# Optimization experiments

Measured on AMD Instinct MI355X. Metric: run time of the kernel, lower is better.

Reference implementation:

```python
import jax, jax.numpy as jnp
import numpy as np

V_CNT = 10000
B = 16
N = B * V_CNT          # total nodes
K = 6                  # Chebyshev order
CH = [3, 128, 64, 32, 128]
G = 8                  # GroupNorm groups (divides 128, 64, 32)
EPS = 1e-5
AVG_DEG = 16


def setup_inputs() -> dict:
    key = jax.random.key(0)
    ks = jax.random.split(key, 8)
    n_edges = N * AVG_DEG
    inp = {
        "x": jax.random.normal(ks[0], (N, CH[0]), jnp.float32),
        "edge_index": jax.random.randint(ks[1], (2, n_edges), 0, N, jnp.int32).astype(jnp.int64),
    }
    for l in range(3):
        cin, cout = CH[l], CH[l + 1]
        s = (1.0 / (cin * K)) ** 0.5
        inp[f"W{l}"] = jax.random.uniform(ks[2 + l], (K, cin, cout), jnp.float32, -s, s)
        inp[f"b{l}"] = jnp.zeros((cout,), jnp.float32)
        inp[f"gamma{l}"] = jnp.ones((cout,), jnp.float32)
        inp[f"beta{l}"] = jnp.zeros((cout,), jnp.float32)
    din = V_CNT * CH[3]
    s = (1.0 / din) ** 0.5
    inp["W_last"] = jax.random.uniform(ks[5], (din, CH[4]), jnp.float32, -s, s)
    inp["b_last"] = jnp.zeros((CH[4],), jnp.float32)
    return inp


def _cheb_edge_weights(edge_index):
    # PyG ChebConv sym normalization with lambda_max=2: L_hat = L - I = -D^{-1/2} A D^{-1/2}
    row, col = edge_index[0], edge_index[1]
    deg = jax.ops.segment_sum(jnp.ones(row.shape, jnp.float32), row, num_segments=N)
    dis = jnp.where(deg > 0, jax.lax.rsqrt(jnp.maximum(deg, 1.0)), 0.0)  # deg^{-1/2}, inf->0
    return -dis[row] * dis[col], row, col


def _cheb_conv(x, row, col, w, W, b):
    # Chebyshev recursion: Tx0=x, Tx1=L_hat x, Tx_k = 2 L_hat Tx_{k-1} - Tx_{k-2}
    prop = lambda h: jax.ops.segment_sum(w[:, None] * h[col], row, num_segments=N)
    Tx0 = x
    out = Tx0 @ W[0]
    Tx1 = prop(Tx0)
    out = out + Tx1 @ W[1]
    for k in range(2, W.shape[0]):
        Tx2 = 2.0 * prop(Tx1) - Tx0
        out = out + Tx2 @ W[k]
        Tx0, Tx1 = Tx1, Tx2
    return out + b


def _group_norm(h, gamma, beta):
    n, C = h.shape
    hg = h.reshape(n, G, C // G)
    mu = hg.mean(axis=2, keepdims=True)
    var = hg.var(axis=2, keepdims=True)
    hg = (hg - mu) * jax.lax.rsqrt(var + EPS)
    return hg.reshape(n, C) * gamma + beta


def reference(x, edge_index, W0, b0, gamma0, beta0, W1, b1, gamma1, beta1,
              W2, b2, gamma2, beta2, W_last, b_last):
    w, row, col = _cheb_edge_weights(edge_index)
    Ws = [W0, W1, W2]
    bs = [b0, b1, b2]
    gs = [gamma0, gamma1, gamma2]
    betas = [beta0, beta1, beta2]
    h = x
    for l in range(3):
        h = _cheb_conv(h, row, col, w, Ws[l], bs[l])
        h = _group_norm(h, gs[l], betas[l])
        h = jax.nn.relu(h)
    h = h.reshape(-1, V_CNT * CH[3])  # [B, v_cnt*32]
    return h @ W_last + b_last
```

## Files before the change

kernel.cpp:

```cpp
#include <hip/hip_runtime.h>
#include <hip/hip_fp16.h>


#define NN 160000
#define EE 2560000
#define FD2 256
#define NBKT 625
#define BCAPL 13

typedef __attribute__((ext_vector_type(8))) _Float16 half8;
typedef __attribute__((ext_vector_type(4))) float floatx4;

__device__ inline float2 h2f2(unsigned u) {
  __half2 h = __builtin_bit_cast(__half2, u);
  return __half22float2(h);
}
__device__ inline unsigned short f2h(float f) {
  return __builtin_bit_cast(unsigned short, __float2half_rn(f));
}
__device__ inline unsigned packh2(float a, float b) {
  return __builtin_bit_cast(unsigned, __floats2half2_rn(a, b));
}

__global__ __launch_bounds__(256) void k_zero(int* __restrict__ p, int n) {
  int i = blockIdx.x * 256 + threadIdx.x;
  if (i < n) p[i] = 0;
}

__global__ __launch_bounds__(256) void k_binit(int* __restrict__ bcur) {
  int i = blockIdx.x * 256 + threadIdx.x;
  if (i < NBKT) bcur[i] = i << BCAPL;
}

__global__ __launch_bounds__(256) void k_bucketA(const int* __restrict__ ei, int* __restrict__ deg,
                                                 int* __restrict__ bcur, int2* __restrict__ stg) {
  __shared__ int bcnt[NBKT];
  __shared__ int gbase[NBKT];
  int tid = threadIdx.x;
  for (int i = tid; i < NBKT; i += 256) bcnt[i] = 0;
  __syncthreads();
  int r[20];
  int e0 = blockIdx.x * 5120;
#pragma unroll
  for (int k = 0; k < 20; k++) {
    int e = e0 + k * 256 + tid;
    int rr = ei[e];
    r[k] = rr;
    atomicAdd(&deg[rr], 1);
    atomicAdd(&bcnt[rr >> 8], 1);
  }
  __syncthreads();
  for (int i = tid; i < NBKT; i += 256) {
    gbase[i] = atomicAdd(&bcur[i], bcnt[i]);
    bcnt[i] = 0;
  }
  __syncthreads();
#pragma unroll
  for (int k = 0; k < 20; k++) {
    int e = e0 + k * 256 + tid;
    int c = ei[EE + e];
    int b = r[k] >> 8;
    int off = atomicAdd(&bcnt[b], 1);
    int pos = gbase[b] + off;
    if (pos < ((b + 1) << BCAPL)) stg[pos] = make_int2(r[k], c);
  }
}

__global__ __launch_bounds__(256) void k_bucketB(const int2* __restrict__ stg, const int* __restrict__ bcur,
                                                 const int* __restrict__ rowStart, const float* __restrict__ dis,
                                                 int2* __restrict__ ew) {
  __shared__ int curs[256];
  int b = blockIdx.x;
  int tid = threadIdx.x;
  int r0 = b << 8;
  curs[tid] = rowStart[r0 + tid];
  __syncthreads();
  int cnt = bcur[b] - (b << BCAPL);
  if (cnt > (1 << BCAPL)) cnt = 1 << BCAPL;
  int base = b << BCAPL;
  for (int k = tid; k < cnt; k += 256) {
    int2 rc = stg[base + k];
    int pos = atomicAdd(&curs[rc.x - r0], 1);
    float w = -dis[rc.x] * dis[rc.y];
    ew[pos] = make_int2(rc.y, __float_as_int(w));
  }
}

__global__ __launch_bounds__(256) void k_dis(const int* __restrict__ deg, float* __restrict__ dis) {
  int i = blockIdx.x * 256 + threadIdx.x;
  if (i < NN) { int d = deg[i]; dis[i] = d > 0 ? rsqrtf((float)d) : 0.f; }
}

__global__ __launch_bounds__(256) void k_scan1(const int* __restrict__ deg, int* __restrict__ rowStart,
                                               int* __restrict__ bsum) {
  __shared__ int s[256];
  int tid = threadIdx.x;
  int i = blockIdx.x * 256 + tid;
  int v = deg[i];
  s[tid] = v;
  __syncthreads();
  for (int off = 1; off < 256; off <<= 1) {
    int t = (tid >= off) ? s[tid - off] : 0;
    __syncthreads();
    s[tid] += t;
    __syncthreads();
  }
  rowStart[i] = s[tid] - v;
  if (tid == 255) bsum[blockIdx.x] = s[255];
}

__global__ void k_scan2(int* __restrict__ bsum, int nb) {
  __shared__ int s[1024];
  int tid = threadIdx.x;
  int v = (tid < nb) ? bsum[tid] : 0;
  s[tid] = v;
  __syncthreads();
  for (int off = 1; off < 1024; off <<= 1) {
    int t = (tid >= off) ? s[tid - off] : 0;
    __syncthreads();
    s[tid] += t;
    __syncthreads();
  }
  if (tid < nb) bsum[tid] = s[tid] - v;
}

__global__ __launch_bounds__(256) void k_scan3(int* __restrict__ rowStart, const int* __restrict__ bsum) {
  int i = blockIdx.x * 256 + threadIdx.x;
  rowStart[i] += bsum[blockIdx.x];
  if (i == 0) rowStart[NN] = EE;
}

__global__ __launch_bounds__(256) void k_copyx(const float* __restrict__ x, float* __restrict__ A,
                                               unsigned short* __restrict__ TxAll) {
  int i = blockIdx.x * 256 + threadIdx.x;
  if (i >= NN) return;
  float v0 = x[i * 3], v1 = x[i * 3 + 1], v2 = x[i * 3 + 2];
  A[i * 3] = v0; A[i * 3 + 1] = v1; A[i * 3 + 2] = v2;
  uint4* dst = reinterpret_cast<uint4*>(TxAll + (size_t)i * 32);
  uint4 z = make_uint4(0u, 0u, 0u, 0u);
  dst[0] = make_uint4(packh2(v0, v1), (unsigned)f2h(v2), 0u, 0u);
  dst[1] = z; dst[2] = z; dst[3] = z;
}

template <int MODE>
__global__ __launch_bounds__(256) void k_prop3(const float* __restrict__ Tsrc, float* __restrict__ Tdst,
                                               unsigned short* __restrict__ TxAll, int ks,
                                               const int* __restrict__ rowStart, const int2* __restrict__ ew) {
  int i = blockIdx.x * 256 + threadIdx.x;
  if (i >= NN) return;
  float a0 = 0.f, a1 = 0.f, a2 = 0.f;
  int e = rowStart[i], e1 = rowStart[i + 1];
  for (; e + 3 < e1; e += 4) {
    int2 p0 = ew[e], p1 = ew[e + 1], p2 = ew[e + 2], p3 = ew[e + 3];
    float w0 = __int_as_float(p0.y), w1 = __int_as_float(p1.y);
    float w2 = __int_as_float(p2.y), w3 = __int_as_float(p3.y);
    a0 += w0 * Tsrc[p0.x * 3] + w1 * Tsrc[p1.x * 3] + w2 * Tsrc[p2.x * 3] + w3 * Tsrc[p3.x * 3];
    a1 += w0 * Tsrc[p0.x * 3 + 1] + w1 * Tsrc[p1.x * 3 + 1] + w2 * Tsrc[p2.x * 3 + 1] + w3 * Tsrc[p3.x * 3 + 1];
    a2 += w0 * Tsrc[p0.x * 3 + 2] + w1 * Tsrc[p1.x * 3 + 2] + w2 * Tsrc[p2.x * 3 + 2] + w3 * Tsrc[p3.x * 3 + 2];
  }
  for (; e < e1; e++) {
    int2 p0 = ew[e];
    float w0 = __int_as_float(p0.y);
    a0 += w0 * Tsrc[p0.x * 3];
    a1 += w0 * Tsrc[p0.x * 3 + 1];
    a2 += w0 * Tsrc[p0.x * 3 + 2];
  }
  if (MODE == 2) {
    a0 = 2.f * a0 - Tdst[i * 3];
    a1 = 2.f * a1 - Tdst[i * 3 + 1];
    a2 = 2.f * a2 - Tdst[i * 3 + 2];
  }
  Tdst[i * 3] = a0; Tdst[i * 3 + 1] = a1; Tdst[i * 3 + 2] = a2;
  unsigned short* tp = TxAll + i * 32 + ks * 3;
  tp[0] = f2h(a0); tp[1] = f2h(a1); tp[2] = f2h(a2);
}

__global__ __launch_bounds__(256) void k_padW0(const float* __restrict__ W0, unsigned short* __restrict__ Bt) {
  int idx = blockIdx.x * 256 + threadIdx.x;
  if (idx >= 128 * 32) return;
  int co = idx >> 5, t = idx & 31;
  Bt[co * 32 + t] = (t < 18) ? f2h(W0[t * 128 + co]) : (unsigned short)0;
}

template <int CIN, int COUT>
__global__ __launch_bounds__(256) void k_combine(const float* __restrict__ W, unsigned short* __restrict__ Bt) {
  int idx = blockIdx.x * 256 + threadIdx.x;
  if (idx >= CIN * 6 * COUT) return;
  int co = idx % COUT;
  int j  = (idx / COUT) % 6;
  int ci = idx / (6 * COUT);
  float c0, c1, c2, c3, c4, c5;
  switch (j) {
    case 0:  c0 = 1;  c1 = 0;  c2 = -1; c3 = 0;   c4 = 1;  c5 = 0;   break;
    case 1:  c0 = 0;  c1 = 1;  c2 = 0;  c3 = -3;  c4 = 0;  c5 = 5;   break;
    case 2:  c0 = 0;  c1 = 0;  c2 = 2;  c3 = 0;   c4 = -8; c5 = 0;   break;
    case 3:  c0 = 0;  c1 = 0;  c2 = 0;  c3 = 4;   c4 = 0;  c5 = -20; break;
    case 4:  c0 = 0;  c1 = 0;  c2 = 0;  c3 = 0;   c4 = 8;  c5 = 0;   break;
    default: c0 = 0;  c1 = 0;  c2 = 0;  c3 = 0;   c4 = 0;  c5 = 16;  break;
  }
  float s = 0.f;
  s += c0 * W[(0 * CIN + ci) * COUT + co];
  s += c1 * W[(1 * CIN + ci) * COUT + co];
  s += c2 * W[(2 * CIN + ci) * COUT + co];
  s += c3 * W[(3 * CIN + ci) * COUT + co];
  s += c4 * W[(4 * CIN + ci) * COUT + co];
  s += c5 * W[(5 * CIN + ci) * COUT + co];
  Bt[(j * COUT + co) * CIN + ci] = f2h(s);
}

template <int KDIM, int COUT>
__global__ __launch_bounds__(256) void k_gemm(const unsigned short* __restrict__ A,
                                              const unsigned short* __restrict__ Bt,
                                              unsigned short* __restrict__ Y) {
  constexpr int KP = KDIM + 8;
  __shared__ unsigned short As[64 * KP];
  __shared__ unsigned short Bs[64 * KP];
  int i0 = blockIdx.x * 64;
  int c0 = blockIdx.y * 64;
  for (int idx = threadIdx.x; idx < 64 * (KDIM / 8); idx += 256) {
    int row = idx / (KDIM / 8), seg = idx % (KDIM / 8);
    uint4 v = ((const uint4*)A)[(size_t)(i0 + row) * (KDIM / 8) + seg];
    *reinterpret_cast<uint4*>(&As[row * KP + seg * 8]) = v;
  }
  for (int idx = threadIdx.x; idx < 64 * (KDIM / 8); idx += 256) {
    int row = idx / (KDIM / 8), seg = idx % (KDIM / 8);
    uint4 v = ((const uint4*)Bt)[(size_t)(c0 + row) * (KDIM / 8) + seg];
    *reinterpret_cast<uint4*>(&Bs[row * KP + seg * 8]) = v;
  }
  __syncthreads();
  int w = threadIdx.x >> 6, lane = threadIdx.x & 63;
  int mn = lane & 15, q = lane >> 4;
  floatx4 acc[4];
#pragma unroll
  for (int cb = 0; cb < 4; cb++) acc[cb] = {0.f, 0.f, 0.f, 0.f};
#pragma unroll
  for (int ks = 0; ks < KDIM / 32; ks++) {
    half8 af = *reinterpret_cast<const half8*>(&As[(16 * w + mn) * KP + ks * 32 + q * 8]);
#pragma unroll
    for (int cb = 0; cb < 4; cb++) {
      half8 bf = *reinterpret_cast<const half8*>(&Bs[(cb * 16 + mn) * KP + ks * 32 + q * 8]);
      acc[cb] = __builtin_amdgcn_mfma_f32_16x16x32_f16(af, bf, acc[cb], 0, 0, 0);
    }
  }
#pragma unroll
  for (int cb = 0; cb < 4; cb++) {
    int jc = c0 + cb * 16 + mn;
    int slice = jc / COUT, cc = jc % COUT;
    unsigned short* dst = Y + (size_t)slice * NN * COUT + cc;
#pragma unroll
    for (int r = 0; r < 4; r++) {
      int i = i0 + 16 * w + q * 4 + r;
      dst[(size_t)i * COUT] = f2h(acc[cb][r]);
    }
  }
}

template <int CPN>
__global__ __launch_bounds__(256) void k_horner(const unsigned* __restrict__ Ysrc, unsigned* __restrict__ Ydst,
                                                const int* __restrict__ rowStart, const int2* __restrict__ ew) {
  int t = blockIdx.x * 256 + threadIdx.x;
  int i = t / CPN;
  int cp = t % CPN;
  float2 a = h2f2(Ydst[(size_t)i * CPN + cp]);
  float acc0 = a.x, acc1 = a.y;
  int e = rowStart[i], e1 = rowStart[i + 1];
  for (; e + 7 < e1; e += 8) {
    int2 p[8];
    unsigned u[8];
#pragma unroll
    for (int k = 0; k < 8; k++) p[k] = ew[e + k];
#pragma unroll
    for (int k = 0; k < 8; k++) u[k] = Ysrc[(size_t)p[k].x * CPN + cp];
#pragma unroll
    for (int k = 0; k < 8; k++) {
      float w = __int_as_float(p[k].y);
      float2 f = h2f2(u[k]);
      acc0 += w * f.x;
      acc1 += w * f.y;
    }
  }
  for (; e < e1; e++) {
    int2 p0 = ew[e];
    float w0 = __int_as_float(p0.y);
    float2 f0 = h2f2(Ysrc[(size_t)p0.x * CPN + cp]);
    acc0 += w0 * f0.x;
    acc1 += w0 * f0.y;
  }
  Ydst[(size_t)i * CPN + cp] = packh2(acc0, acc1);
}

template <int CPG>
__global__ __launch_bounds__(256) void k_gn(const unsigned short* __restrict__ src, const float* __restrict__ bias,
                                            const float* __restrict__ gamma, const float* __restrict__ beta,
                                            unsigned short* __restrict__ dst) {
  constexpr int C = CPG * 8;
  int t = blockIdx.x * 256 + threadIdx.x;
  int i = t >> 3, g = t & 7;
  float v[CPG];
  const unsigned* p = reinterpret_cast<const unsigned*>(src + (size_t)i * C + g * CPG);
#pragma unroll
  for (int q = 0; q < CPG / 2; q++) {
    float2 f = h2f2(p[q]);
    v[2 * q] = f.x; v[2 * q + 1] = f.y;
  }
  float mean = 0.f;
#pragma unroll
  for (int c = 0; c < CPG; c++) { v[c] += bias[g * CPG + c]; mean += v[c]; }
  mean *= (1.f / CPG);
  float var = 0.f;
#pragma unroll
  for (int c = 0; c < CPG; c++) { float d = v[c] - mean; var += d * d; }
  var *= (1.f / CPG);
  float rs = rsqrtf(var + 1e-5f);
  unsigned* dp = reinterpret_cast<unsigned*>(dst + (size_t)i * C + g * CPG);
#pragma unroll
  for (int q = 0; q < CPG / 2; q++) {
    float o0 = fmaxf((v[2 * q] - mean) * rs * gamma[g * CPG + 2 * q] + beta[g * CPG + 2 * q], 0.f);
    float o1 = fmaxf((v[2 * q + 1] - mean) * rs * gamma[g * CPG + 2 * q + 1] + beta[g * CPG + 2 * q + 1], 0.f);
    dp[q] = packh2(o0, o1);
  }
}

__global__ __launch_bounds__(256) void k_final1(const unsigned short* __restrict__ h3,
                                                const float* __restrict__ Wl,
                                                float* __restrict__ part) {
  __shared__ float hs[16 * FD2];
  __shared__ float red[2048];
  int d0 = blockIdx.x * FD2;
  const unsigned* h3u = reinterpret_cast<const unsigned*>(h3);
  for (int idx = threadIdx.x; idx < 16 * (FD2 / 2); idx += 256) {
    int b = idx / (FD2 / 2), dq = idx % (FD2 / 2);
    float2 f = h2f2(h3u[(size_t)b * 160000 + (d0 >> 1) + dq]);
    hs[b * FD2 + 2 * dq] = f.x;
    hs[b * FD2 + 2 * dq + 1] = f.y;
  }
  __syncthreads();
  int w = threadIdx.x >> 6, lane = threadIdx.x & 63;
  float a0[16], a1[16];
#pragma unroll
  for (int b = 0; b < 16; b++) { a0[b] = 0.f; a1[b] = 0.f; }
  const float* wp = Wl + (size_t)(d0 + w * (FD2 / 4)) * 128 + 2 * lane;
#pragma unroll 2
  for (int r = 0; r < FD2 / 4; r++) {
    float2 wv = *reinterpret_cast<const float2*>(wp + (size_t)r * 128);
    int row = w * (FD2 / 4) + r;
#pragma unroll
    for (int b = 0; b < 16; b++) {
      float h = hs[b * FD2 + row];
      a0[b] += wv.x * h;
      a1[b] += wv.y * h;
    }
  }
  float2* red2 = reinterpret_cast<float2*>(red);
  for (int ww = 0; ww < 4; ww++) {
    if (w == ww) {
#pragma unroll
      for (int b = 0; b < 16; b++) {
        if (ww == 0) {
          red2[b * 64 + lane] = make_float2(a0[b], a1[b]);
        } else {
          float2 r2 = red2[b * 64 + lane];
          r2.x += a0[b]; r2.y += a1[b];
          red2[b * 64 + lane] = r2;
        }
      }
    }
    __syncthreads();
  }
  for (int i = threadIdx.x; i < 2048; i += 256)
    part[(size_t)blockIdx.x * 2048 + i] = red[i];
}

__global__ __launch_bounds__(256) void k_final2(const float* __restrict__ part, const float* __restrict__ bl,
                                                float* __restrict__ out) {
  int o = blockIdx.x * 256 + threadIdx.x;
  float s = bl[o & 127];
#pragma unroll 10
  for (int p = 0; p < 1250; p++) s += part[(size_t)p * 2048 + o];
  out[o] = s;
}

extern "C" void kernel_launch(void* const* d_in, const int* in_sizes, int n_in,
                              void* d_out, int out_size, void* d_ws, size_t ws_size,
                              hipStream_t stream) {
  const float* x   = (const float*)d_in[0];
  const int*   ei  = (const int*)d_in[1];
  const float* W0  = (const float*)d_in[2];
  const float* b0  = (const float*)d_in[3];
  const float* g0  = (const float*)d_in[4];
  const float* be0 = (const float*)d_in[5];
  const float* W1  = (const float*)d_in[6];
  const float* b1  = (const float*)d_in[7];
  const float* g1  = (const float*)d_in[8];
  const float* be1 = (const float*)d_in[9];
  const float* W2  = (const float*)d_in[10];
  const float* b2  = (const float*)d_in[11];
  const float* g2  = (const float*)d_in[12];
  const float* be2 = (const float*)d_in[13];
  const float* Wl  = (const float*)d_in[14];
  const float* bl  = (const float*)d_in[15];
  float* out = (float*)d_out;
  (void)in_sizes; (void)n_in; (void)out_size; (void)ws_size;

  char* pw = (char*)d_ws;
  auto carve = [&](size_t bytes) -> void* {
    void* r = (void*)pw;
    pw += (bytes + 255) & ~(size_t)255;
    return r;
  };
  int*            deg      = (int*)   carve((size_t)NN * 4);
  int*            bcur     = (int*)   carve((size_t)NBKT * 4);
  int*            rowStart = (int*)   carve((size_t)(NN + 1) * 4);
  int*            bsum     = (int*)   carve(1024 * 4);
  float*          dis      = (float*) carve((size_t)NN * 4);
  int2*           ew       = (int2*)  carve((size_t)EE * 8);
  unsigned short* Cwt      = (unsigned short*)carve((size_t)384 * 128 * 2);
  unsigned short* TxAll    = (unsigned short*)carve((size_t)NN * 32 * 2);
  float*          A3       = (float*) carve((size_t)NN * 3 * 4);
  float*          B3       = (float*) carve((size_t)NN * 3 * 4);
  unsigned short* Hbuf     = (unsigned short*)carve((size_t)NN * 128 * 2);
  unsigned short* Ybuf     = (unsigned short*)carve((size_t)NN * 384 * 2);
  float*          part     = (float*) carve((size_t)1250 * 2048 * 4);
  int2*           stg      = (int2*)Ybuf;

  k_zero<<<625, 256, 0, stream>>>(deg, NN);
  k_binit<<<3, 256, 0, stream>>>(bcur);
  k_bucketA<<<500, 256, 0, stream>>>(ei, deg, bcur, stg);
  k_dis<<<625, 256, 0, stream>>>(deg, dis);
  k_scan1<<<625, 256, 0, stream>>>(deg, rowStart, bsum);
  k_scan2<<<1, 1024, 0, stream>>>(bsum, 625);
  k_scan3<<<625, 256, 0, stream>>>(rowStart, bsum);
  k_bucketB<<<NBKT, 256, 0, stream>>>(stg, bcur, rowStart, dis, ew);

  k_copyx<<<625, 256, 0, stream>>>(x, A3, TxAll);
  k_prop3<1><<<625, 256, 0, stream>>>(A3, B3, TxAll, 1, rowStart, ew);
  k_prop3<2><<<625, 256, 0, stream>>>(B3, A3, TxAll, 2, rowStart, ew);
  k_prop3<2><<<625, 256, 0, stream>>>(A3, B3, TxAll, 3, rowStart, ew);
  k_prop3<2><<<625, 256, 0, stream>>>(B3, A3, TxAll, 4, rowStart, ew);
  k_prop3<2><<<625, 256, 0, stream>>>(A3, B3, TxAll, 5, rowStart, ew);
  k_padW0<<<16, 256, 0, stream>>>(W0, Cwt);
  k_gemm<32, 128><<<dim3(2500, 2), 256, 0, stream>>>(TxAll, Cwt, Ybuf);
  k_gn<16><<<5000, 256, 0, stream>>>(Ybuf, b0, g0, be0, Hbuf);

  k_combine<128, 64><<<192, 256, 0, stream>>>(W1, Cwt);
  k_gemm<128, 64><<<dim3(2500, 6), 256, 0, stream>>>(Hbuf, Cwt, Ybuf);
  for (int j = 4; j >= 0; j--)
    k_horner<32><<<20000, 256, 0, stream>>>((unsigned*)(Ybuf + (size_t)(j + 1) * NN * 64),
                                            (unsigned*)(Ybuf + (size_t)j * NN * 64), rowStart, ew);
  k_gn<8><<<5000, 256, 0, stream>>>(Ybuf, b1, g1, be1, Hbuf);

  k_combine<64, 32><<<48, 256, 0, stream>>>(W2, Cwt);
  k_gemm<64, 32><<<dim3(2500, 3), 256, 0, stream>>>(Hbuf, Cwt, Ybuf);
  for (int j = 4; j >= 0; j--)
    k_horner<16><<<10000, 256, 0, stream>>>((unsigned*)(Ybuf + (size_t)(j + 1) * NN * 32),
                                            (unsigned*)(Ybuf + (size_t)j * NN * 32), rowStart, ew);
  k_gn<4><<<5000, 256, 0, stream>>>(Ybuf, b2, g2, be2, Hbuf);

  k_final1<<<1250, 256, 0, stream>>>(Hbuf, Wl, part);
  k_final2<<<8, 256, 0, stream>>>(part, bl, out);
}
```

Measured before the change: 1.370 ms.

## Compress CSR edges to column-only and factor normalization into gather kernels

The CSR edge array now stores only the 4-byte column index instead of a column/weight pair. The edge weight is rebuilt from dis[col] inside the propagation and Horner kernels, and -dis[row] is applied once per row after the sum. Staging entries are packed into 32 bits by keeping the low 8 row bits next to the 18-bit column. The bucketing kernel runs fewer blocks with more edges each and rereads row indices instead of holding them in registers. This halves edge-array traffic on the gather-heavy passes, at the cost of an extra random dis lookup per edge, which should mostly hit cache.

```diff
diff --git a/kernel.cpp b/kernel.cpp
--- a/kernel.cpp
+++ b/kernel.cpp
@@ -7,6 +7,8 @@
 #define FD2 256
 #define NBKT 625
 #define BCAPL 13
+#define ABLK 200
+#define EPT 50
 
 typedef __attribute__((ext_vector_type(8))) _Float16 half8;
 typedef __attribute__((ext_vector_type(4))) float floatx4;
@@ -33,19 +35,17 @@
 }
 
 __global__ __launch_bounds__(256) void k_bucketA(const int* __restrict__ ei, int* __restrict__ deg,
-                                                 int* __restrict__ bcur, int2* __restrict__ stg) {
+                                                 int* __restrict__ bcur, unsigned* __restrict__ stg) {
   __shared__ int bcnt[NBKT];
   __shared__ int gbase[NBKT];
   int tid = threadIdx.x;
   for (int i = tid; i < NBKT; i += 256) bcnt[i] = 0;
   __syncthreads();
-  int r[20];
-  int e0 = blockIdx.x * 5120;
-#pragma unroll
-  for (int k = 0; k < 20; k++) {
+  int e0 = blockIdx.x * (256 * EPT);
+#pragma unroll 5
+  for (int k = 0; k < EPT; k++) {
     int e = e0 + k * 256 + tid;
     int rr = ei[e];
-    r[k] = rr;
     atomicAdd(&deg[rr], 1);
     atomicAdd(&bcnt[rr >> 8], 1);
   }
@@ -55,20 +55,21 @@
     bcnt[i] = 0;
   }
   __syncthreads();
-#pragma unroll
-  for (int k = 0; k < 20; k++) {
+#pragma unroll 5
+  for (int k = 0; k < EPT; k++) {
     int e = e0 + k * 256 + tid;
+    int rr = ei[e];
     int c = ei[EE + e];
-    int b = r[k] >> 8;
+    int b = rr >> 8;
     int off = atomicAdd(&bcnt[b], 1);
     int pos = gbase[b] + off;
-    if (pos < ((b + 1) << BCAPL)) stg[pos] = make_int2(r[k], c);
-  }
-}
-
-__global__ __launch_bounds__(256) void k_bucketB(const int2* __restrict__ stg, const int* __restrict__ bcur,
-                                                 const int* __restrict__ rowStart, const float* __restrict__ dis,
-                                                 int2* __restrict__ ew) {
+    if (pos < ((b + 1) << BCAPL))
+      stg[pos] = ((unsigned)(rr & 255) << 18) | (unsigned)c;
+  }
+}
+
+__global__ __launch_bounds__(256) void k_bucketB(const unsigned* __restrict__ stg, const int* __restrict__ bcur,
+                                                 const int* __restrict__ rowStart, unsigned* __restrict__ ewc) {
   __shared__ int curs[256];
   int b = blockIdx.x;
   int tid = threadIdx.x;
@@ -79,10 +80,10 @@
   if (cnt > (1 << BCAPL)) cnt = 1 << BCAPL;
   int base = b << BCAPL;
   for (int k = tid; k < cnt; k += 256) {
-    int2 rc = stg[base + k];
-    int pos = atomicAdd(&curs[rc.x - r0], 1);
-    float w = -dis[rc.x] * dis[rc.y];
-    ew[pos] = make_int2(rc.y, __float_as_int(w));
+    unsigned u = stg[base + k];
+    int rlow = u >> 18;
+    int pos = atomicAdd(&curs[rlow], 1);
+    ewc[pos] = u & 0x3FFFFu;
   }
 }
 
@@ -145,26 +146,28 @@
 template <int MODE>
 __global__ __launch_bounds__(256) void k_prop3(const float* __restrict__ Tsrc, float* __restrict__ Tdst,
                                                unsigned short* __restrict__ TxAll, int ks,
-                                               const int* __restrict__ rowStart, const int2* __restrict__ ew) {
+                                               const int* __restrict__ rowStart, const unsigned* __restrict__ ewc,
+                                               const float* __restrict__ dis) {
   int i = blockIdx.x * 256 + threadIdx.x;
   if (i >= NN) return;
-  float a0 = 0.f, a1 = 0.f, a2 = 0.f;
+  float s0 = 0.f, s1 = 0.f, s2 = 0.f;
   int e = rowStart[i], e1 = rowStart[i + 1];
   for (; e + 3 < e1; e += 4) {
-    int2 p0 = ew[e], p1 = ew[e + 1], p2 = ew[e + 2], p3 = ew[e + 3];
-    float w0 = __int_as_float(p0.y), w1 = __int_as_float(p1.y);
-    float w2 = __int_as_float(p2.y), w3 = __int_as_float(p3.y);
-    a0 += w0 * Tsrc[p0.x * 3] + w1 * Tsrc[p1.x * 3] + w2 * Tsrc[p2.x * 3] + w3 * Tsrc[p3.x * 3];
-    a1 += w0 * Tsrc[p0.x * 3 + 1] + w1 * Tsrc[p1.x * 3 + 1] + w2 * Tsrc[p2.x * 3 + 1] + w3 * Tsrc[p3.x * 3 + 1];
-    a2 += w0 * Tsrc[p0.x * 3 + 2] + w1 * Tsrc[p1.x * 3 + 2] + w2 * Tsrc[p2.x * 3 + 2] + w3 * Tsrc[p3.x * 3 + 2];
+    unsigned c0 = ewc[e], c1 = ewc[e + 1], c2 = ewc[e + 2], c3 = ewc[e + 3];
+    float w0 = dis[c0], w1 = dis[c1], w2 = dis[c2], w3 = dis[c3];
+    s0 += w0 * Tsrc[c0 * 3] + w1 * Tsrc[c1 * 3] + w2 * Tsrc[c2 * 3] + w3 * Tsrc[c3 * 3];
+    s1 += w0 * Tsrc[c0 * 3 + 1] + w1 * Tsrc[c1 * 3 + 1] + w2 * Tsrc[c2 * 3 + 1] + w3 * Tsrc[c3 * 3 + 1];
+    s2 += w0 * Tsrc[c0 * 3 + 2] + w1 * Tsrc[c1 * 3 + 2] + w2 * Tsrc[c2 * 3 + 2] + w3 * Tsrc[c3 * 3 + 2];
   }
   for (; e < e1; e++) {
-    int2 p0 = ew[e];
-    float w0 = __int_as_float(p0.y);
-    a0 += w0 * Tsrc[p0.x * 3];
-    a1 += w0 * Tsrc[p0.x * 3 + 1];
-    a2 += w0 * Tsrc[p0.x * 3 + 2];
-  }
+    unsigned c0 = ewc[e];
+    float w0 = dis[c0];
+    s0 += w0 * Tsrc[c0 * 3];
+    s1 += w0 * Tsrc[c0 * 3 + 1];
+    s2 += w0 * Tsrc[c0 * 3 + 2];
+  }
+  float di = -dis[i];
+  float a0 = di * s0, a1 = di * s1, a2 = di * s2;
   if (MODE == 2) {
     a0 = 2.f * a0 - Tdst[i * 3];
     a1 = 2.f * a1 - Tdst[i * 3 + 1];
@@ -257,36 +260,40 @@
 
 template <int CPN>
 __global__ __launch_bounds__(256) void k_horner(const unsigned* __restrict__ Ysrc, unsigned* __restrict__ Ydst,
-                                                const int* __restrict__ rowStart, const int2* __restrict__ ew) {
+                                                const int* __restrict__ rowStart, const unsigned* __restrict__ ewc,
+                                                const float* __restrict__ dis) {
   int t = blockIdx.x * 256 + threadIdx.x;
   int i = t / CPN;
   int cp = t % CPN;
   float2 a = h2f2(Ydst[(size_t)i * CPN + cp]);
-  float acc0 = a.x, acc1 = a.y;
+  float s0 = 0.f, s1 = 0.f;
   int e = rowStart[i], e1 = rowStart[i + 1];
   for (; e + 7 < e1; e += 8) {
-    int2 p[8];
+    unsigned cc[8];
+    float wv[8];
     unsigned u[8];
 #pragma unroll
-    for (int k = 0; k < 8; k++) p[k] = ew[e + k];
-#pragma unroll
-    for (int k = 0; k < 8; k++) u[k] = Ysrc[(size_t)p[k].x * CPN + cp];
+    for (int k = 0; k < 8; k++) cc[k] = ewc[e + k];
+#pragma unroll
+    for (int k = 0; k < 8; k++) wv[k] = dis[cc[k]];
+#pragma unroll
+    for (int k = 0; k < 8; k++) u[k] = Ysrc[(size_t)cc[k] * CPN + cp];
 #pragma unroll
     for (int k = 0; k < 8; k++) {
-      float w = __int_as_float(p[k].y);
       float2 f = h2f2(u[k]);
-      acc0 += w * f.x;
-      acc1 += w * f.y;
+      s0 += wv[k] * f.x;
+      s1 += wv[k] * f.y;
     }
   }
   for (; e < e1; e++) {
-    int2 p0 = ew[e];
-    float w0 = __int_as_float(p0.y);
-    float2 f0 = h2f2(Ysrc[(size_t)p0.x * CPN + cp]);
-    acc0 += w0 * f0.x;
-    acc1 += w0 * f0.y;
-  }
-  Ydst[(size_t)i * CPN + cp] = packh2(acc0, acc1);
+    unsigned c0 = ewc[e];
+    float w0 = dis[c0];
+    float2 f0 = h2f2(Ysrc[(size_t)c0 * CPN + cp]);
+    s0 += w0 * f0.x;
+    s1 += w0 * f0.y;
+  }
+  float di = -dis[i];
+  Ydst[(size_t)i * CPN + cp] = packh2(a.x + di * s0, a.y + di * s1);
 }
 
 template <int CPG>
@@ -413,7 +420,7 @@
   int*            rowStart = (int*)   carve((size_t)(NN + 1) * 4);
   int*            bsum     = (int*)   carve(1024 * 4);
   float*          dis      = (float*) carve((size_t)NN * 4);
-  int2*           ew       = (int2*)  carve((size_t)EE * 8);
+  unsigned*       ewc      = (unsigned*)carve((size_t)EE * 4);
   unsigned short* Cwt      = (unsigned short*)carve((size_t)384 * 128 * 2);
   unsigned short* TxAll    = (unsigned short*)carve((size_t)NN * 32 * 2);
   float*          A3       = (float*) carve((size_t)NN * 3 * 4);
@@ -421,23 +428,23 @@
   unsigned short* Hbuf     = (unsigned short*)carve((size_t)NN * 128 * 2);
   unsigned short* Ybuf     = (unsigned short*)carve((size_t)NN * 384 * 2);
   float*          part     = (float*) carve((size_t)1250 * 2048 * 4);
-  int2*           stg      = (int2*)Ybuf;
+  unsigned*       stg      = (unsigned*)Ybuf;
 
   k_zero<<<625, 256, 0, stream>>>(deg, NN);
   k_binit<<<3, 256, 0, stream>>>(bcur);
-  k_bucketA<<<500, 256, 0, stream>>>(ei, deg, bcur, stg);
+  k_bucketA<<<ABLK, 256, 0, stream>>>(ei, deg, bcur, stg);
   k_dis<<<625, 256, 0, stream>>>(deg, dis);
   k_scan1<<<625, 256, 0, stream>>>(deg, rowStart, bsum);
   k_scan2<<<1, 1024, 0, stream>>>(bsum, 625);
   k_scan3<<<625, 256, 0, stream>>>(rowStart, bsum);
-  k_bucketB<<<NBKT, 256, 0, stream>>>(stg, bcur, rowStart, dis, ew);
+  k_bucketB<<<NBKT, 256, 0, stream>>>(stg, bcur, rowStart, ewc);
 
   k_copyx<<<625, 256, 0, stream>>>(x, A3, TxAll);
-  k_prop3<1><<<625, 256, 0, stream>>>(A3, B3, TxAll, 1, rowStart, ew);
-  k_prop3<2><<<625, 256, 0, stream>>>(B3, A3, TxAll, 2, rowStart, ew);
-  k_prop3<2><<<625, 256, 0, stream>>>(A3, B3, TxAll, 3, rowStart, ew);
-  k_prop3<2><<<625, 256, 0, stream>>>(B3, A3, TxAll, 4, rowStart, ew);
-  k_prop3<2><<<625, 256, 0, stream>>>(A3, B3, TxAll, 5, rowStart, ew);
+  k_prop3<1><<<625, 256, 0, stream>>>(A3, B3, TxAll, 1, rowStart, ewc, dis);
+  k_prop3<2><<<625, 256, 0, stream>>>(B3, A3, TxAll, 2, rowStart, ewc, dis);
+  k_prop3<2><<<625, 256, 0, stream>>>(A3, B3, TxAll, 3, rowStart, ewc, dis);
+  k_prop3<2><<<625, 256, 0, stream>>>(B3, A3, TxAll, 4, rowStart, ewc, dis);
+  k_prop3<2><<<625, 256, 0, stream>>>(A3, B3, TxAll, 5, rowStart, ewc, dis);
   k_padW0<<<16, 256, 0, stream>>>(W0, Cwt);
   k_gemm<32, 128><<<dim3(2500, 2), 256, 0, stream>>>(TxAll, Cwt, Ybuf);
   k_gn<16><<<5000, 256, 0, stream>>>(Ybuf, b0, g0, be0, Hbuf);
@@ -446,14 +453,14 @@
   k_gemm<128, 64><<<dim3(2500, 6), 256, 0, stream>>>(Hbuf, Cwt, Ybuf);
   for (int j = 4; j >= 0; j--)
     k_horner<32><<<20000, 256, 0, stream>>>((unsigned*)(Ybuf + (size_t)(j + 1) * NN * 64),
-                                            (unsigned*)(Ybuf + (size_t)j * NN * 64), rowStart, ew);
+                                            (unsigned*)(Ybuf + (size_t)j * NN * 64), rowStart, ewc, dis);
   k_gn<8><<<5000, 256, 0, stream>>>(Ybuf, b1, g1, be1, Hbuf);
 
   k_combine<64, 32><<<48, 256, 0, stream>>>(W2, Cwt);
   k_gemm<64, 32><<<dim3(2500, 3), 256, 0, stream>>>(Hbuf, Cwt, Ybuf);
   for (int j = 4; j >= 0; j--)
     k_horner<16><<<10000, 256, 0, stream>>>((unsigned*)(Ybuf + (size_t)(j + 1) * NN * 32),
-                                            (unsigned*)(Ybuf + (size_t)j * NN * 32), rowStart, ew);
+                                            (unsigned*)(Ybuf + (size_t)j * NN * 32), rowStart, ewc, dis);
   k_gn<4><<<5000, 256, 0, stream>>>(Ybuf, b2, g2, be2, Hbuf);
 
   k_final1<<<1250, 256, 0, stream>>>(Hbuf, Wl, part);
```

Measured after the change: 1.484 ms. 8.3% more time.

## Derive degrees and row offsets from buckets, drop global degree atomics

Applied to the files above, without the earlier changes.

Removes the global per-edge degree atomics and the separate zero, dis and three-pass scan kernels. Degrees are now counted per bucket in shared memory, and row starts come from a single bucket-level scan plus a per-bucket local scan. Staging entries are packed into 32 bits (low 8 row bits plus column), which halves staging traffic, and the edge-weight kernel caches the bucket's dis values in LDS. The cost is a second pass over the staging buffer and a reliance on column indices fitting in 18 bits.

```diff
diff --git a/kernel.cpp b/kernel.cpp
--- a/kernel.cpp
+++ b/kernel.cpp
@@ -7,6 +7,8 @@
 #define FD2 256
 #define NBKT 625
 #define BCAPL 13
+#define ABLK 500
+#define EPT 20
 
 typedef __attribute__((ext_vector_type(8))) _Float16 half8;
 typedef __attribute__((ext_vector_type(4))) float floatx4;
@@ -22,32 +24,25 @@
   return __builtin_bit_cast(unsigned, __floats2half2_rn(a, b));
 }
 
-__global__ __launch_bounds__(256) void k_zero(int* __restrict__ p, int n) {
-  int i = blockIdx.x * 256 + threadIdx.x;
-  if (i < n) p[i] = 0;
-}
-
 __global__ __launch_bounds__(256) void k_binit(int* __restrict__ bcur) {
   int i = blockIdx.x * 256 + threadIdx.x;
   if (i < NBKT) bcur[i] = i << BCAPL;
 }
 
-__global__ __launch_bounds__(256) void k_bucketA(const int* __restrict__ ei, int* __restrict__ deg,
-                                                 int* __restrict__ bcur, int2* __restrict__ stg) {
+__global__ __launch_bounds__(256) void k_bucketA(const int* __restrict__ ei,
+                                                 int* __restrict__ bcur, unsigned* __restrict__ stg) {
   __shared__ int bcnt[NBKT];
   __shared__ int gbase[NBKT];
   int tid = threadIdx.x;
   for (int i = tid; i < NBKT; i += 256) bcnt[i] = 0;
   __syncthreads();
-  int r[20];
-  int e0 = blockIdx.x * 5120;
-#pragma unroll
-  for (int k = 0; k < 20; k++) {
+  int r[EPT];
+  int e0 = blockIdx.x * (256 * EPT);
+#pragma unroll
+  for (int k = 0; k < EPT; k++) {
     int e = e0 + k * 256 + tid;
-    int rr = ei[e];
-    r[k] = rr;
-    atomicAdd(&deg[rr], 1);
-    atomicAdd(&bcnt[rr >> 8], 1);
+    r[k] = ei[e];
+    atomicAdd(&bcnt[r[k] >> 8], 1);
   }
   __syncthreads();
   for (int i = tid; i < NBKT; i += 256) {
@@ -56,48 +51,55 @@
   }
   __syncthreads();
 #pragma unroll
-  for (int k = 0; k < 20; k++) {
+  for (int k = 0; k < EPT; k++) {
     int e = e0 + k * 256 + tid;
     int c = ei[EE + e];
     int b = r[k] >> 8;
     int off = atomicAdd(&bcnt[b], 1);
     int pos = gbase[b] + off;
-    if (pos < ((b + 1) << BCAPL)) stg[pos] = make_int2(r[k], c);
-  }
-}
-
-__global__ __launch_bounds__(256) void k_bucketB(const int2* __restrict__ stg, const int* __restrict__ bcur,
-                                                 const int* __restrict__ rowStart, const float* __restrict__ dis,
-                                                 int2* __restrict__ ew) {
-  __shared__ int curs[256];
+    if (pos < ((b + 1) << BCAPL))
+      stg[pos] = ((unsigned)(r[k] & 255) << 18) | (unsigned)c;
+  }
+}
+
+__global__ void k_bktscan(const int* __restrict__ bcur, int* __restrict__ bbase,
+                          int* __restrict__ rowStart) {
+  __shared__ int s[1024];
+  int tid = threadIdx.x;
+  int tot = 0;
+  if (tid < NBKT) {
+    tot = bcur[tid] - (tid << BCAPL);
+    if (tot > (1 << BCAPL)) tot = 1 << BCAPL;
+  }
+  s[tid] = tot;
+  __syncthreads();
+  for (int off = 1; off < 1024; off <<= 1) {
+    int t = (tid >= off) ? s[tid - off] : 0;
+    __syncthreads();
+    s[tid] += t;
+    __syncthreads();
+  }
+  if (tid < NBKT) bbase[tid] = s[tid] - tot;
+  if (tid == 0) rowStart[NN] = EE;
+}
+
+__global__ __launch_bounds__(256) void k_bucketB1(const unsigned* __restrict__ stg, const int* __restrict__ bcur,
+                                                  const int* __restrict__ bbase, int* __restrict__ rowStart,
+                                                  float* __restrict__ dis) {
+  __shared__ int degl[256];
+  __shared__ int s[256];
   int b = blockIdx.x;
   int tid = threadIdx.x;
-  int r0 = b << 8;
-  curs[tid] = rowStart[r0 + tid];
+  degl[tid] = 0;
   __syncthreads();
   int cnt = bcur[b] - (b << BCAPL);
   if (cnt > (1 << BCAPL)) cnt = 1 << BCAPL;
   int base = b << BCAPL;
-  for (int k = tid; k < cnt; k += 256) {
-    int2 rc = stg[base + k];
-    int pos = atomicAdd(&curs[rc.x - r0], 1);
-    float w = -dis[rc.x] * dis[rc.y];
-    ew[pos] = make_int2(rc.y, __float_as_int(w));
-  }
-}
-
-__global__ __launch_bounds__(256) void k_dis(const int* __restrict__ deg, float* __restrict__ dis) {
-  int i = blockIdx.x * 256 + threadIdx.x;
-  if (i < NN) { int d = deg[i]; dis[i] = d > 0 ? rsqrtf((float)d) : 0.f; }
-}
-
-__global__ __launch_bounds__(256) void k_scan1(const int* __restrict__ deg, int* __restrict__ rowStart,
-                                               int* __restrict__ bsum) {
-  __shared__ int s[256];
-  int tid = threadIdx.x;
-  int i = blockIdx.x * 256 + tid;
-  int v = deg[i];
-  s[tid] = v;
+  for (int k = tid; k < cnt; k += 256)
+    atomicAdd(&degl[stg[base + k] >> 18], 1);
+  __syncthreads();
+  int d = degl[tid];
+  s[tid] = d;
   __syncthreads();
   for (int off = 1; off < 256; off <<= 1) {
     int t = (tid >= off) ? s[tid - off] : 0;
@@ -105,29 +107,33 @@
     s[tid] += t;
     __syncthreads();
   }
-  rowStart[i] = s[tid] - v;
-  if (tid == 255) bsum[blockIdx.x] = s[255];
-}
-
-__global__ void k_scan2(int* __restrict__ bsum, int nb) {
-  __shared__ int s[1024];
+  int r0 = b << 8;
+  rowStart[r0 + tid] = bbase[b] + s[tid] - d;
+  dis[r0 + tid] = d > 0 ? rsqrtf((float)d) : 0.f;
+}
+
+__global__ __launch_bounds__(256) void k_bucketB2(const unsigned* __restrict__ stg, const int* __restrict__ bcur,
+                                                  const int* __restrict__ rowStart, const float* __restrict__ dis,
+                                                  int2* __restrict__ ew) {
+  __shared__ int curs[256];
+  __shared__ float disl[256];
+  int b = blockIdx.x;
   int tid = threadIdx.x;
-  int v = (tid < nb) ? bsum[tid] : 0;
-  s[tid] = v;
-  __syncthreads();
-  for (int off = 1; off < 1024; off <<= 1) {
-    int t = (tid >= off) ? s[tid - off] : 0;
-    __syncthreads();
-    s[tid] += t;
-    __syncthreads();
-  }
-  if (tid < nb) bsum[tid] = s[tid] - v;
-}
-
-__global__ __launch_bounds__(256) void k_scan3(int* __restrict__ rowStart, const int* __restrict__ bsum) {
-  int i = blockIdx.x * 256 + threadIdx.x;
-  rowStart[i] += bsum[blockIdx.x];
-  if (i == 0) rowStart[NN] = EE;
+  int r0 = b << 8;
+  curs[tid] = rowStart[r0 + tid];
+  disl[tid] = dis[r0 + tid];
+  __syncthreads();
+  int cnt = bcur[b] - (b << BCAPL);
+  if (cnt > (1 << BCAPL)) cnt = 1 << BCAPL;
+  int base = b << BCAPL;
+  for (int k = tid; k < cnt; k += 256) {
+    unsigned u = stg[base + k];
+    int rlow = u >> 18;
+    int c = u & 0x3FFFFu;
+    int pos = atomicAdd(&curs[rlow], 1);
+    float w = -disl[rlow] * dis[c];
+    ew[pos] = make_int2(c, __float_as_int(w));
+  }
 }
 
 __global__ __launch_bounds__(256) void k_copyx(const float* __restrict__ x, float* __restrict__ A,
@@ -408,10 +414,9 @@
     pw += (bytes + 255) & ~(size_t)255;
     return r;
   };
-  int*            deg      = (int*)   carve((size_t)NN * 4);
   int*            bcur     = (int*)   carve((size_t)NBKT * 4);
+  int*            bbase    = (int*)   carve((size_t)NBKT * 4);
   int*            rowStart = (int*)   carve((size_t)(NN + 1) * 4);
-  int*            bsum     = (int*)   carve(1024 * 4);
   float*          dis      = (float*) carve((size_t)NN * 4);
   int2*           ew       = (int2*)  carve((size_t)EE * 8);
   unsigned short* Cwt      = (unsigned short*)carve((size_t)384 * 128 * 2);
@@ -421,16 +426,13 @@
   unsigned short* Hbuf     = (unsigned short*)carve((size_t)NN * 128 * 2);
   unsigned short* Ybuf     = (unsigned short*)carve((size_t)NN * 384 * 2);
   float*          part     = (float*) carve((size_t)1250 * 2048 * 4);
-  int2*           stg      = (int2*)Ybuf;
-
-  k_zero<<<625, 256, 0, stream>>>(deg, NN);
+  unsigned*       stg      = (unsigned*)Ybuf;
+
   k_binit<<<3, 256, 0, stream>>>(bcur);
-  k_bucketA<<<500, 256, 0, stream>>>(ei, deg, bcur, stg);
-  k_dis<<<625, 256, 0, stream>>>(deg, dis);
-  k_scan1<<<625, 256, 0, stream>>>(deg, rowStart, bsum);
-  k_scan2<<<1, 1024, 0, stream>>>(bsum, 625);
-  k_scan3<<<625, 256, 0, stream>>>(rowStart, bsum);
-  k_bucketB<<<NBKT, 256, 0, stream>>>(stg, bcur, rowStart, dis, ew);
+  k_bucketA<<<ABLK, 256, 0, stream>>>(ei, bcur, stg);
+  k_bktscan<<<1, 1024, 0, stream>>>(bcur, bbase, rowStart);
+  k_bucketB1<<<NBKT, 256, 0, stream>>>(stg, bcur, bbase, rowStart, dis);
+  k_bucketB2<<<NBKT, 256, 0, stream>>>(stg, bcur, rowStart, dis, ew);
 
   k_copyx<<<625, 256, 0, stream>>>(x, A3, TxAll);
   k_prop3<1><<<625, 256, 0, stream>>>(A3, B3, TxAll, 1, rowStart, ew);
```

Result: faster. 1.281 ms (-6.5%).
